# Kernel optimization log

Hardware: AMD Instinct MI355X
Metric: run time of the kernel (lower is better)

The kernel has to match this reference:

```python
import jax, jax.numpy as jnp
import numpy as np

# ---- static config (mirrors GptOssDecoderLayer init) ----
H = 1024      # hidden_size
HD = 64       # head_size
NQ = 16       # num_query_heads
NKV = 4       # num_key_value_heads
G = NQ // NKV # num_key_value_groups
E = 8         # num_experts
TOPK = 2      # experts_per_token
FFN = 1024    # expert intermediate (== hidden in GPT-OSS)
B, Q = 4, 128 # batch sequences, new query tokens per sequence
P, PS = 8, 128
S = P * PS    # kv length per sequence
T = B * Q     # total query tokens
SW = 128      # sliding window (layer_idx % 2 == 0 -> active)
LIMIT = 7.0   # swiglu_limit
ALPHA = 1.702
EPS = 1e-5
NEG = -1e30
SCALE = HD ** -0.5


def rmsnorm(x, w):
    return x * w * jax.lax.rsqrt(jnp.mean(x * x, axis=-1, keepdims=True) + EPS)


def setup_inputs() -> dict:
    key = jax.random.key(0)
    ks = jax.random.split(key, 16)
    hidden = jax.random.normal(ks[0], (T, H), jnp.float32)
    kv_cache = jax.random.normal(ks[1], (B * P, 2, PS, NKV, HD), jnp.float32)
    kv_page_indices = jnp.arange(B * P, dtype=jnp.int32).reshape(B, P)
    # additive causal mask: query q sits at absolute position S - Q + q
    qpos = S - Q + jnp.arange(Q)
    kpos = jnp.arange(S)
    causal = qpos[:, None] >= kpos[None, :]
    attention_mask = jnp.broadcast_to(
        jnp.where(causal, 0.0, NEG).astype(jnp.float32), (B, Q, S))
    sinks = 0.1 * jax.random.normal(ks[2], (NQ,), jnp.float32)
    w_qkv = jax.random.normal(ks[3], (H, HD * (NQ + 2 * NKV)), jnp.float32) / np.sqrt(H)
    b_qkv = jnp.zeros((HD * (NQ + 2 * NKV),), jnp.float32)
    w_o = jax.random.normal(ks[4], (NQ * HD, H), jnp.float32) / np.sqrt(NQ * HD)
    b_o = jnp.zeros((H,), jnp.float32)
    ln1_w = jnp.ones((H,), jnp.float32)
    ln2_w = jnp.ones((H,), jnp.float32)
    w_router = jax.random.normal(ks[5], (H, E), jnp.float32) / np.sqrt(H)
    b_router = jnp.zeros((E,), jnp.float32)
    w_gate_up = jax.random.normal(ks[6], (E, H, 2 * FFN), jnp.float32) / np.sqrt(H)
    b_gate_up = jnp.zeros((E, 2 * FFN), jnp.float32)
    w_down = jax.random.normal(ks[7], (E, FFN, H), jnp.float32) / np.sqrt(FFN)
    b_down = jnp.zeros((E, H), jnp.float32)
    return dict(hidden=hidden, kv_cache=kv_cache, attention_mask=attention_mask,
                kv_page_indices=kv_page_indices, sinks=sinks, w_qkv=w_qkv,
                b_qkv=b_qkv, w_o=w_o, b_o=b_o, ln1_w=ln1_w, ln2_w=ln2_w,
                w_router=w_router, b_router=b_router, w_gate_up=w_gate_up,
                b_gate_up=b_gate_up, w_down=w_down, b_down=b_down)


def reference(hidden, kv_cache, attention_mask, kv_page_indices, sinks,
              w_qkv, b_qkv, w_o, b_o, ln1_w, ln2_w, w_router, b_router,
              w_gate_up, b_gate_up, w_down, b_down):
    # ---- attention block ----
    x = rmsnorm(hidden, ln1_w)
    qkv = x @ w_qkv + b_qkv                       # [T, HD*(NQ+2*NKV)]
    q = qkv[:, :NQ * HD].reshape(B, Q, NQ, HD)
    k_new = qkv[:, NQ * HD:(NQ + NKV) * HD].reshape(B, Q, NKV, HD)
    v_new = qkv[:, (NQ + NKV) * HD:].reshape(B, Q, NKV, HD)
    # gather paged KV cache -> [B, S, NKV, HD]; write new tokens into tail slots
    pages = kv_cache[kv_page_indices]             # [B, P, 2, PS, NKV, HD]
    K = pages[:, :, 0].reshape(B, S, NKV, HD).at[:, S - Q:].set(k_new)
    V = pages[:, :, 1].reshape(B, S, NKV, HD).at[:, S - Q:].set(v_new)
    Kr = jnp.repeat(K, G, axis=2)                 # GQA expand -> [B, S, NQ, HD]
    Vr = jnp.repeat(V, G, axis=2)
    scores = jnp.einsum('bqhd,bshd->bhqs', q * SCALE, Kr) + attention_mask[:, None]
    # sliding-window (module trims pages outside the window; equivalent mask)
    qpos = S - Q + jnp.arange(Q)
    kpos = jnp.arange(S)
    win_ok = (qpos[:, None] - kpos[None, :]) < SW
    scores = jnp.where(win_ok[None, None], scores, NEG)
    m = jnp.max(scores, axis=-1)
    m = jnp.where(jnp.isinf(m) & (m < 0), 0.0, m)
    p = jnp.exp(scores - m[..., None])            # [B, NQ, Q, S]
    # attention sink joins the softmax denominator (online-softmax correction)
    denom = jnp.sum(p, axis=-1) + jnp.exp(sinks[None, :, None] - m)
    attn = jnp.einsum('bhqs,bshd->bhqd', p, Vr) / denom[..., None]
    attn = attn.transpose(0, 2, 1, 3).reshape(T, NQ * HD)
    h = hidden + attn @ w_o + b_o
    # ---- MoE block ----
    x2 = rmsnorm(h, ln2_w)
    logits = x2 @ w_router + b_router             # [T, E]
    vals, idx = jax.lax.top_k(logits, TOPK)
    wts = jax.nn.softmax(vals, axis=-1)
    comb = jnp.sum(jax.nn.one_hot(idx, E, dtype=x2.dtype) * wts[..., None], axis=1)
    gu = jnp.einsum('th,ehf->etf', x2, w_gate_up) + b_gate_up[:, None, :]
    gate = jnp.minimum(gu[..., 0::2], LIMIT)
    up = jnp.clip(gu[..., 1::2], -LIMIT, LIMIT)
    glu = gate * jax.nn.sigmoid(gate * ALPHA)
    eo = jnp.einsum('etf,efh->eth', (up + 1.0) * glu, w_down) + b_down[:, None, :]
    moe = jnp.einsum('te,eth->th', comb, eo)
    return h + moe
```

## Files before the change

### kernel.cpp

```cpp
#include <hip/hip_runtime.h>

constexpr int H    = 1024;
constexpr int HD   = 64;
constexpr int NQ   = 16;
constexpr int NKV  = 4;
constexpr int E_   = 8;
constexpr int FFN  = 1024;
constexpr int B_   = 4;
constexpr int Q_   = 128;
constexpr int P_   = 8;
constexpr int PS   = 128;
constexpr int S_   = P_ * PS;
constexpr int T_   = B_ * Q_;
constexpr int QKV_N = HD * (NQ + 2 * NKV);
constexpr float EPS   = 1e-5f;
constexpr float ALPHA = 1.702f;
constexpr float LIMIT = 7.0f;
constexpr float SCALE = 0.125f;

constexpr int MAXROWS = 1536;
constexpr int MAXTILES = 24;

typedef __attribute__((ext_vector_type(4))) float f32x4;
typedef __attribute__((ext_vector_type(8))) short s16x8;

__device__ __forceinline__ unsigned short f2bf(float f) {
    unsigned u = __float_as_uint(f);
    u += 0x7FFFu + ((u >> 16) & 1u);
    return (unsigned short)(u >> 16);
}

__global__ __launch_bounds__(256) void rmsnorm_kernel(const float* __restrict__ in,
                                                      const float* __restrict__ w,
                                                      unsigned short* __restrict__ outb,
                                                      int* __restrict__ cnt) {
    int t   = blockIdx.x;
    int tid = threadIdx.x;
    if (t == 0 && tid < E_) cnt[tid] = 0;
    float4 v = ((const float4*)(in + (size_t)t * H))[tid];
    float ss = v.x * v.x + v.y * v.y + v.z * v.z + v.w * v.w;
#pragma unroll
    for (int off = 32; off; off >>= 1) ss += __shfl_down(ss, off);
    __shared__ float partial[4];
    __shared__ float s_inv;
    if ((tid & 63) == 0) partial[tid >> 6] = ss;
    __syncthreads();
    if (tid == 0)
        s_inv = rsqrtf((partial[0] + partial[1] + partial[2] + partial[3]) * (1.0f / H) + EPS);
    __syncthreads();
    float inv = s_inv;
    float4 wv = ((const float4*)w)[tid];
    ushort4 ob;
    ob.x = f2bf(v.x * wv.x * inv); ob.y = f2bf(v.y * wv.y * inv);
    ob.z = f2bf(v.z * wv.z * inv); ob.w = f2bf(v.w * wv.w * inv);
    ((ushort4*)(outb + (size_t)t * H))[tid] = ob;
}

__global__ __launch_bounds__(256, 4) void gemm_dense_t(const unsigned short* __restrict__ Abf,
                                                       const float* __restrict__ W,
                                                       const float* __restrict__ bias,
                                                       const float* __restrict__ resid,
                                                       float* __restrict__ C,
                                                       float* __restrict__ Cdup, int N) {
    int nb = blockIdx.x, mb = blockIdx.y * 64;
    int tid = threadIdx.x;
    int w = tid >> 6, lane = tid & 63;
    int r16 = lane & 15, kq = lane >> 4;
    int skb = tid >> 5, sn = tid & 31;

    __shared__ unsigned short Wt[2][8][32][8];

    size_t sN = (size_t)N;
    const float* wsrc = W + (size_t)(skb * 8) * sN + nb * 32 + sn;
    const unsigned short* ap = Abf + (size_t)(mb + w * 16 + r16) * 1024 + kq * 8;

    float wr[2][8];
    s16x8 af[2][2];
    f32x4 acc[2] = {};

#pragma unroll
    for (int j = 0; j < 8; j++) wr[0][j] = wsrc[(size_t)j * sN];
    {
        s16x8 p;
#pragma unroll
        for (int j = 0; j < 8; j++) p[j] = (short)f2bf(wr[0][j]);
        *(s16x8*)&Wt[0][skb][sn][0] = p;
    }
#pragma unroll
    for (int j = 0; j < 8; j++) wr[1][j] = wsrc[(size_t)(64 + j) * sN];
#pragma unroll
    for (int ks = 0; ks < 2; ks++) af[0][ks] = *(const s16x8*)(ap + ks * 32);
    __syncthreads();

#pragma unroll
    for (int t = 0; t < 16; t++) {
        s16x8 b0[2], b1[2];
#pragma unroll
        for (int ks = 0; ks < 2; ks++) {
            b0[ks] = *(const s16x8*)&Wt[t & 1][ks * 4 + kq][r16][0];
            b1[ks] = *(const s16x8*)&Wt[t & 1][ks * 4 + kq][16 + r16][0];
        }
        if (t < 15) {
#pragma unroll
            for (int ks = 0; ks < 2; ks++)
                af[(t + 1) & 1][ks] = *(const s16x8*)(ap + (t + 1) * 64 + ks * 32);
        }
        if (t < 14) {
#pragma unroll
            for (int j = 0; j < 8; j++) wr[t & 1][j] = wsrc[(size_t)((t + 2) * 64 + j) * sN];
        }
#pragma unroll
        for (int ks = 0; ks < 2; ks++) {
            acc[0] = __builtin_amdgcn_mfma_f32_16x16x32_bf16(af[t & 1][ks], b0[ks], acc[0], 0, 0, 0);
            acc[1] = __builtin_amdgcn_mfma_f32_16x16x32_bf16(af[t & 1][ks], b1[ks], acc[1], 0, 0, 0);
        }
        if (t < 15) {
            s16x8 p;
#pragma unroll
            for (int j = 0; j < 8; j++) p[j] = (short)f2bf(wr[(t + 1) & 1][j]);
            *(s16x8*)&Wt[(t + 1) & 1][skb][sn][0] = p;
        }
        __syncthreads();
    }

    int row0 = mb + w * 16 + kq * 4;
#pragma unroll
    for (int nf = 0; nf < 2; nf++) {
        int col = nb * 32 + nf * 16 + r16;
        float bcol = bias[col];
#pragma unroll
        for (int r = 0; r < 4; r++) {
            int row = row0 + r;
            float v = acc[nf][r] + bcol;
            if (resid) v += resid[(size_t)row * sN + col];
            C[(size_t)row * sN + col] = v;
            if (Cdup) Cdup[(size_t)row * sN + col] = v;
        }
    }
}

__global__ __launch_bounds__(256) void attn_group_kernel(const float* __restrict__ qkv,
                                                         const float* __restrict__ kv_cache,
                                                         const int* __restrict__ page_idx,
                                                         const float* __restrict__ sinks,
                                                         unsigned short* __restrict__ attn_bf) {
    int blk = blockIdx.x;
    int kvh = blk & 3;
    int q   = (blk >> 2) & 127;
    int b   = blk >> 9;
    int t   = b * Q_ + q;
    int tid = threadIdx.x;
    int s_lo = S_ - Q_ - 127 + q;

    __shared__ __align__(16) float Vs[128][64];
    __shared__ __align__(16) float qs4[4][64];
    __shared__ float pv[4][128];
    __shared__ float sD[4];

#pragma unroll
    for (int r = 0; r < 8; r++) {
        int l = r * 256 + tid;
        int key = l >> 4, c = l & 15;
        int s = s_lo + key;
        const float* vp;
        if (s < S_ - Q_) {
            int page = page_idx[b * P_ + (s >> 7)];
            vp = kv_cache + (size_t)page * 65536 + 32768 + (size_t)(s & 127) * (NKV * HD) + kvh * HD;
        } else {
            vp = qkv + (size_t)(b * Q_ + (s - (S_ - Q_))) * QKV_N + (NQ + NKV) * HD + kvh * HD;
        }
        ((float4*)Vs[key])[c] = *(const float4*)(vp + c * 4);
    }
    {
        int hh = tid >> 6, d2 = tid & 63;
        qs4[hh][d2] = qkv[(size_t)t * QKV_N + (kvh * 4 + hh) * HD + d2];
    }
    __syncthreads();

    {
        int key = tid & 127, hp = tid >> 7;
        int s = s_lo + key;
        const float* kp;
        if (s < S_ - Q_) {
            int page = page_idx[b * P_ + (s >> 7)];
            kp = kv_cache + (size_t)page * 65536 + (size_t)(s & 127) * (NKV * HD) + kvh * HD;
        } else {
            kp = qkv + (size_t)(b * Q_ + (s - (S_ - Q_))) * QKV_N + NQ * HD + kvh * HD;
        }
        const float4* kp4 = (const float4*)kp;
        const float4* q0p = (const float4*)qs4[hp * 2];
        const float4* q1p = (const float4*)qs4[hp * 2 + 1];
        float sc0 = 0.f, sc1 = 0.f;
#pragma unroll
        for (int d4 = 0; d4 < 16; d4++) {
            float4 kk = kp4[d4];
            float4 q0 = q0p[d4], q1 = q1p[d4];
            sc0 += q0.x * kk.x + q0.y * kk.y + q0.z * kk.z + q0.w * kk.w;
            sc1 += q1.x * kk.x + q1.y * kk.y + q1.z * kk.z + q1.w * kk.w;
        }
        pv[hp * 2][key]     = sc0 * SCALE;
        pv[hp * 2 + 1][key] = sc1 * SCALE;
    }
    __syncthreads();

    {
        int wv = tid >> 6, lane = tid & 63;
        float a0 = pv[wv][lane], a1 = pv[wv][lane + 64];
        float m = fmaxf(a0, a1);
#pragma unroll
        for (int off = 32; off; off >>= 1) m = fmaxf(m, __shfl_xor(m, off));
        float p0 = __expf(a0 - m), p1 = __expf(a1 - m);
        float l = p0 + p1;
#pragma unroll
        for (int off = 32; off; off >>= 1) l += __shfl_xor(l, off);
        pv[wv][lane] = p0;
        pv[wv][lane + 64] = p1;
        if (lane == 0) sD[wv] = l + __expf(sinks[kvh * 4 + wv] - m);
    }
    __syncthreads();

    {
        int hh = tid >> 6, d2 = tid & 63;
        float a0 = 0.f, a1 = 0.f, a2 = 0.f, a3 = 0.f;
#pragma unroll 4
        for (int i = 0; i < 128; i += 4) {
            a0 += pv[hh][i]     * Vs[i][d2];
            a1 += pv[hh][i + 1] * Vs[i + 1][d2];
            a2 += pv[hh][i + 2] * Vs[i + 2][d2];
            a3 += pv[hh][i + 3] * Vs[i + 3][d2];
        }
        float acc = ((a0 + a1) + (a2 + a3)) / sD[hh];
        attn_bf[(size_t)t * (NQ * HD) + (kvh * 4 + hh) * HD + d2] = f2bf(acc);
    }
}

__global__ __launch_bounds__(256) void rms_router_kernel(const float* __restrict__ hbuf,
                                                         const float* __restrict__ ln2w,
                                                         const float* __restrict__ w_router,
                                                         const float* __restrict__ b_router,
                                                         unsigned short* __restrict__ x2bf,
                                                         int* __restrict__ ridx,
                                                         float* __restrict__ rwt,
                                                         int* __restrict__ cnt) {
    int t = blockIdx.x;
    int tid = threadIdx.x;
    float4 v = ((const float4*)(hbuf + (size_t)t * H))[tid];
    float ss = v.x * v.x + v.y * v.y + v.z * v.z + v.w * v.w;
#pragma unroll
    for (int off = 32; off; off >>= 1) ss += __shfl_down(ss, off);
    __shared__ float partial[4];
    __shared__ float s_inv;
    if ((tid & 63) == 0) partial[tid >> 6] = ss;
    __syncthreads();
    if (tid == 0)
        s_inv = rsqrtf((partial[0] + partial[1] + partial[2] + partial[3]) * (1.0f / H) + EPS);
    __syncthreads();
    float inv = s_inv;
    float4 wv = ((const float4*)ln2w)[tid];
    float4 o;
    o.x = v.x * wv.x * inv; o.y = v.y * wv.y * inv;
    o.z = v.z * wv.z * inv; o.w = v.w * wv.w * inv;
    ushort4 ob;
    ob.x = f2bf(o.x); ob.y = f2bf(o.y); ob.z = f2bf(o.z); ob.w = f2bf(o.w);
    ((ushort4*)(x2bf + (size_t)t * H))[tid] = ob;

    const float4* wr = (const float4*)(w_router + (size_t)tid * 4 * E_);
    float p[E_];
    {
        float4 r0a = wr[0], r0b = wr[1];
        float4 r1a = wr[2], r1b = wr[3];
        float4 r2a = wr[4], r2b = wr[5];
        float4 r3a = wr[6], r3b = wr[7];
        p[0] = o.x * r0a.x + o.y * r1a.x + o.z * r2a.x + o.w * r3a.x;
        p[1] = o.x * r0a.y + o.y * r1a.y + o.z * r2a.y + o.w * r3a.y;
        p[2] = o.x * r0a.z + o.y * r1a.z + o.z * r2a.z + o.w * r3a.z;
        p[3] = o.x * r0a.w + o.y * r1a.w + o.z * r2a.w + o.w * r3a.w;
        p[4] = o.x * r0b.x + o.y * r1b.x + o.z * r2b.x + o.w * r3b.x;
        p[5] = o.x * r0b.y + o.y * r1b.y + o.z * r2b.y + o.w * r3b.y;
        p[6] = o.x * r0b.z + o.y * r1b.z + o.z * r2b.z + o.w * r3b.z;
        p[7] = o.x * r0b.w + o.y * r1b.w + o.z * r2b.w + o.w * r3b.w;
    }
    __shared__ float wsum[4][E_];
    int wv2 = tid >> 6, lane = tid & 63;
#pragma unroll
    for (int e = 0; e < E_; e++) {
        float r = p[e];
#pragma unroll
        for (int off = 32; off; off >>= 1) r += __shfl_xor(r, off);
        if (lane == 0) wsum[wv2][e] = r;
    }
    __syncthreads();
    __shared__ float logits[E_];
    if (tid < E_)
        logits[tid] = wsum[0][tid] + wsum[1][tid] + wsum[2][tid] + wsum[3][tid] + b_router[tid];
    __syncthreads();
    if (tid == 0) {
        int i0 = 0; float v0 = logits[0];
        for (int ee = 1; ee < E_; ee++)
            if (logits[ee] > v0) { v0 = logits[ee]; i0 = ee; }
        int i1 = -1; float v1 = -3.4e38f;
        for (int ee = 0; ee < E_; ee++)
            if (ee != i0 && logits[ee] > v1) { v1 = logits[ee]; i1 = ee; }
        float w0 = 1.0f / (1.0f + __expf(v1 - v0));
        ridx[t * 2] = i0; ridx[t * 2 + 1] = i1;
        rwt[t * 2] = w0;  rwt[t * 2 + 1] = 1.0f - w0;
        atomicAdd(&cnt[i0], 1);
        atomicAdd(&cnt[i1], 1);
    }
}

__global__ __launch_bounds__(256) void plumb_kernel(const int* __restrict__ cnt,
                                                    const int* __restrict__ ridx,
                                                    int* __restrict__ poff,
                                                    int* __restrict__ list,
                                                    int* __restrict__ tmap) {
    __shared__ int lpos[E_], lpoff[E_];
    int tid = threadIdx.x;
    if (tid == 0) {
        int run = 0, it = 0;
        for (int e = 0; e < E_; e++) {
            lpoff[e] = run; poff[e] = run;
            int pc = (cnt[e] + 63) & ~63;
            for (int tl = 0; tl < (pc >> 6); tl++) tmap[1 + it++] = (e << 5) | tl;
            run += pc;
        }
        tmap[0] = it;
    }
    if (tid < E_) lpos[tid] = 0;
    __syncthreads();
    for (int i = tid; i < 2 * T_; i += 256) {
        int e = ridx[i];
        int pp = atomicAdd(&lpos[e], 1);
        list[lpoff[e] + pp] = i;
    }
}

__global__ __launch_bounds__(256, 4) void moe_gateup_t(const unsigned short* __restrict__ x2bf,
                                                       const int* __restrict__ list,
                                                       const int* __restrict__ cnt,
                                                       const int* __restrict__ poff,
                                                       const int* __restrict__ tmap,
                                                       const float* __restrict__ wgu,
                                                       const float* __restrict__ bgu,
                                                       unsigned short* __restrict__ act_bf) {
    if ((int)blockIdx.y >= tmap[0]) return;
    int v0m = tmap[1 + blockIdx.y];
    int e = v0m >> 5, tl = v0m & 31;
    int n = cnt[e];
    int base = poff[e];
    int nb = blockIdx.x;
    int tid = threadIdx.x;
    int w = tid >> 6, lane = tid & 63;
    int r16 = lane & 15, kq = lane >> 4;
    int skb = tid >> 5, sn = tid & 31;

    __shared__ unsigned short Wt[2][8][32][8];

    const float* wsrc = wgu + (size_t)e * (1024 * 2048) + (size_t)(skb * 8) * 2048 + nb * 32 + sn;
    int rr0 = tl * 64 + w * 16 + r16;
    int t2a = (rr0 < n) ? list[base + rr0] : list[base];
    const unsigned short* ap = x2bf + (size_t)(t2a >> 1) * 1024 + kq * 8;

    float wr[2][8];
    s16x8 af[2][2];
    f32x4 acc[2] = {};

#pragma unroll
    for (int j = 0; j < 8; j++) wr[0][j] = wsrc[(size_t)j * 2048];
    {
        s16x8 p;
#pragma unroll
        for (int j = 0; j < 8; j++) p[j] = (short)f2bf(wr[0][j]);
        *(s16x8*)&Wt[0][skb][sn][0] = p;
    }
#pragma unroll
    for (int j = 0; j < 8; j++) wr[1][j] = wsrc[(size_t)(64 + j) * 2048];
#pragma unroll
    for (int ks = 0; ks < 2; ks++) af[0][ks] = *(const s16x8*)(ap + ks * 32);
    __syncthreads();

#pragma unroll
    for (int t = 0; t < 16; t++) {
        s16x8 b0[2], b1[2];
#pragma unroll
        for (int ks = 0; ks < 2; ks++) {
            b0[ks] = *(const s16x8*)&Wt[t & 1][ks * 4 + kq][r16][0];
            b1[ks] = *(const s16x8*)&Wt[t & 1][ks * 4 + kq][16 + r16][0];
        }
        if (t < 15) {
#pragma unroll
            for (int ks = 0; ks < 2; ks++)
                af[(t + 1) & 1][ks] = *(const s16x8*)(ap + (t + 1) * 64 + ks * 32);
        }
        if (t < 14) {
#pragma unroll
            for (int j = 0; j < 8; j++) wr[t & 1][j] = wsrc[(size_t)((t + 2) * 64 + j) * 2048];
        }
#pragma unroll
        for (int ks = 0; ks < 2; ks++) {
            acc[0] = __builtin_amdgcn_mfma_f32_16x16x32_bf16(af[t & 1][ks], b0[ks], acc[0], 0, 0, 0);
            acc[1] = __builtin_amdgcn_mfma_f32_16x16x32_bf16(af[t & 1][ks], b1[ks], acc[1], 0, 0, 0);
        }
        if (t < 15) {
            s16x8 p;
#pragma unroll
            for (int j = 0; j < 8; j++) p[j] = (short)f2bf(wr[(t + 1) & 1][j]);
            *(s16x8*)&Wt[(t + 1) & 1][skb][sn][0] = p;
        }
        __syncthreads();
    }

    int parity = r16 & 1;
#pragma unroll
    for (int nf = 0; nf < 2; nf++) {
        int gucol = nb * 32 + nf * 16 + r16;
        float bb = bgu[(size_t)e * 2048 + gucol];
#pragma unroll
        for (int r = 0; r < 4; r++) {
            float v = acc[nf][r] + bb;
            float o = __shfl_xor(v, 1);
            if (!parity) {
                float g = fminf(v, LIMIT);
                float u = fminf(fmaxf(o, -LIMIT), LIMIT);
                float glu = g / (1.0f + __expf(-ALPHA * g));
                int rr = tl * 64 + w * 16 + kq * 4 + r;
                if (rr < n)
                    act_bf[(size_t)(base + rr) * FFN + (gucol >> 1)] = f2bf((u + 1.0f) * glu);
            }
        }
    }
}

__global__ __launch_bounds__(256, 4) void moe_down_t(const unsigned short* __restrict__ act_bf,
                                                     const int* __restrict__ list,
                                                     const int* __restrict__ cnt,
                                                     const int* __restrict__ poff,
                                                     const int* __restrict__ tmap,
                                                     const float* __restrict__ rwt,
                                                     const float* __restrict__ wdn,
                                                     const float* __restrict__ b_down,
                                                     float* __restrict__ out) {
    if ((int)blockIdx.y >= tmap[0]) return;
    int v0m = tmap[1 + blockIdx.y];
    int e = v0m >> 5, tl = v0m & 31;
    int n = cnt[e];
    int base = poff[e];
    int nb = blockIdx.x;
    int z  = blockIdx.z;
    int tid = threadIdx.x;
    int w = tid >> 6, lane = tid & 63;
    int r16 = lane & 15, kq = lane >> 4;
    int skb = tid >> 5, sn = tid & 31;

    __shared__ unsigned short Wt[2][8][32][8];

    const float* wsrc = wdn + (size_t)e * (1024 * 1024) + (size_t)(z * 512 + skb * 8) * 1024 + nb * 32 + sn;
    const unsigned short* ap = act_bf + (size_t)(base + tl * 64 + w * 16 + r16) * 1024 + z * 512 + kq * 8;

    float wr[2][8];
    s16x8 af[2][2];
    f32x4 acc[2] = {};

#pragma unroll
    for (int j = 0; j < 8; j++) wr[0][j] = wsrc[(size_t)j * 1024];
    {
        s16x8 p;
#pragma unroll
        for (int j = 0; j < 8; j++) p[j] = (short)f2bf(wr[0][j]);
        *(s16x8*)&Wt[0][skb][sn][0] = p;
    }
#pragma unroll
    for (int j = 0; j < 8; j++) wr[1][j] = wsrc[(size_t)(64 + j) * 1024];
#pragma unroll
    for (int ks = 0; ks < 2; ks++) af[0][ks] = *(const s16x8*)(ap + ks * 32);
    __syncthreads();

#pragma unroll
    for (int t = 0; t < 8; t++) {
        s16x8 b0[2], b1[2];
#pragma unroll
        for (int ks = 0; ks < 2; ks++) {
            b0[ks] = *(const s16x8*)&Wt[t & 1][ks * 4 + kq][r16][0];
            b1[ks] = *(const s16x8*)&Wt[t & 1][ks * 4 + kq][16 + r16][0];
        }
        if (t < 7) {
#pragma unroll
            for (int ks = 0; ks < 2; ks++)
                af[(t + 1) & 1][ks] = *(const s16x8*)(ap + (t + 1) * 64 + ks * 32);
        }
        if (t < 6) {
#pragma unroll
            for (int j = 0; j < 8; j++) wr[t & 1][j] = wsrc[(size_t)((t + 2) * 64 + j) * 1024];
        }
#pragma unroll
        for (int ks = 0; ks < 2; ks++) {
            acc[0] = __builtin_amdgcn_mfma_f32_16x16x32_bf16(af[t & 1][ks], b0[ks], acc[0], 0, 0, 0);
            acc[1] = __builtin_amdgcn_mfma_f32_16x16x32_bf16(af[t & 1][ks], b1[ks], acc[1], 0, 0, 0);
        }
        if (t < 7) {
            s16x8 p;
#pragma unroll
            for (int j = 0; j < 8; j++) p[j] = (short)f2bf(wr[(t + 1) & 1][j]);
            *(s16x8*)&Wt[(t + 1) & 1][skb][sn][0] = p;
        }
        __syncthreads();
    }

#pragma unroll
    for (int r = 0; r < 4; r++) {
        int rr = tl * 64 + w * 16 + kq * 4 + r;
        if (rr < n) {
            int t2 = list[base + rr];
            float sc = rwt[t2];
            float* op = out + (size_t)(t2 >> 1) * H;
#pragma unroll
            for (int nf = 0; nf < 2; nf++) {
                int col = nb * 32 + nf * 16 + r16;
                float v = acc[nf][r] + (z == 0 ? b_down[(size_t)e * 1024 + col] : 0.0f);
                atomicAdd(op + col, sc * v);
            }
        }
    }
}

extern "C" void kernel_launch(void* const* d_in, const int* in_sizes, int n_in,
                              void* d_out, int out_size, void* d_ws, size_t ws_size,
                              hipStream_t stream) {
    const float* hidden          = (const float*)d_in[0];
    const float* kv_cache        = (const float*)d_in[1];
    const int*   kv_page_indices = (const int*)d_in[3];
    const float* sinks           = (const float*)d_in[4];
    const float* w_qkv           = (const float*)d_in[5];
    const float* b_qkv           = (const float*)d_in[6];
    const float* w_o             = (const float*)d_in[7];
    const float* b_o             = (const float*)d_in[8];
    const float* ln1_w           = (const float*)d_in[9];
    const float* ln2_w           = (const float*)d_in[10];
    const float* w_router        = (const float*)d_in[11];
    const float* b_router        = (const float*)d_in[12];
    const float* w_gate_up       = (const float*)d_in[13];
    const float* b_gate_up       = (const float*)d_in[14];
    const float* w_down          = (const float*)d_in[15];
    const float* b_down          = (const float*)d_in[16];
    float* out = (float*)d_out;

    char* base = (char*)d_ws;
    float* qkv   = (float*)base;                       base += (size_t)T_ * QKV_N * 4;
    float* hbuf  = (float*)base;                       base += (size_t)T_ * H * 4;
    unsigned short* x_bf    = (unsigned short*)base;   base += (size_t)T_ * H * 2;
    unsigned short* x2_bf   = (unsigned short*)base;   base += (size_t)T_ * H * 2;
    unsigned short* attn_bf = (unsigned short*)base;   base += (size_t)T_ * NQ * HD * 2;
    unsigned short* act_bf  = (unsigned short*)base;   base += (size_t)(MAXROWS + 128) * FFN * 2;
    float* rwt  = (float*)base;                        base += 2 * T_ * 4;
    int*   ridx = (int*)base;                          base += 2 * T_ * 4;
    int*   cnt  = (int*)base;                          base += E_ * 4;
    int*   poff = (int*)base;                          base += E_ * 4;
    int*   list = (int*)base;                          base += MAXROWS * 4;
    int*   tmap = (int*)base;                          base += (1 + MAXTILES + 7) * 4;

    rmsnorm_kernel<<<T_, 256, 0, stream>>>(hidden, ln1_w, x_bf, cnt);
    gemm_dense_t<<<dim3(QKV_N / 32, T_ / 64), 256, 0, stream>>>(
        x_bf, w_qkv, b_qkv, nullptr, qkv, nullptr, QKV_N);
    attn_group_kernel<<<B_ * Q_ * NKV, 256, 0, stream>>>(qkv, kv_cache, kv_page_indices, sinks, attn_bf);
    gemm_dense_t<<<dim3(H / 32, T_ / 64), 256, 0, stream>>>(
        attn_bf, w_o, b_o, hidden, hbuf, out, H);
    rms_router_kernel<<<T_, 256, 0, stream>>>(hbuf, ln2_w, w_router, b_router,
                                              x2_bf, ridx, rwt, cnt);
    plumb_kernel<<<1, 256, 0, stream>>>(cnt, ridx, poff, list, tmap);
    moe_gateup_t<<<dim3(FFN * 2 / 32, MAXTILES), 256, 0, stream>>>(
        x2_bf, list, cnt, poff, tmap, w_gate_up, b_gate_up, act_bf);
    moe_down_t<<<dim3(H / 32, MAXTILES, 2), 256, 0, stream>>>(
        act_bf, list, cnt, poff, tmap, rwt, w_down, b_down, out);
}
```

Before: 274.7 us.

## Deepen weight prefetch pipeline to four stages with explicit LDS barriers

Restructures the three bf16 MFMA GEMM kernels (dense, MoE gate-up, MoE down) so global weight loads are issued four k-tiles ahead, using rotating register buffers and named ping-pong LDS tiles. __syncthreads is replaced by a custom barrier that waits only on LDS counters, so in-flight global loads are not drained at each step. The occupancy hint is dropped from launch_bounds to make room for the extra registers. This aims to hide global memory latency on the fp32 weight stream, at the cost of higher register pressure and possibly lower occupancy.

Result: no change. 278.0 us (+1.2%).

```diff
diff --git a/kernel.cpp b/kernel.cpp
--- a/kernel.cpp
+++ b/kernel.cpp
@@ -30,6 +30,11 @@
     return (unsigned short)(u >> 16);
 }
 
+__device__ __forceinline__ void lds_barrier() {
+    asm volatile("s_waitcnt lgkmcnt(0)" ::: "memory");
+    __builtin_amdgcn_s_barrier();
+}
+
 __global__ __launch_bounds__(256) void rmsnorm_kernel(const float* __restrict__ in,
                                                       const float* __restrict__ w,
                                                       unsigned short* __restrict__ outb,
@@ -56,74 +61,88 @@
     ((ushort4*)(outb + (size_t)t * H))[tid] = ob;
 }
 
-__global__ __launch_bounds__(256, 4) void gemm_dense_t(const unsigned short* __restrict__ Abf,
-                                                       const float* __restrict__ W,
-                                                       const float* __restrict__ bias,
-                                                       const float* __restrict__ resid,
-                                                       float* __restrict__ C,
-                                                       float* __restrict__ Cdup, int N) {
+#define GPHASE(LDSR, LDSW, WRW, WRI, TI, NT, AFD0, AFD1, TA, AFS0, AFS1, STRIDE)      \
+    {                                                                                  \
+        s16x8 b00 = *(const s16x8*)&LDSR[kq][r16][0];                                  \
+        s16x8 b01 = *(const s16x8*)&LDSR[kq][16 + r16][0];                             \
+        s16x8 b10 = *(const s16x8*)&LDSR[4 + kq][r16][0];                              \
+        s16x8 b11 = *(const s16x8*)&LDSR[4 + kq][16 + r16][0];                         \
+        if (TA < NT) {                                                                 \
+            AFD0 = *(const s16x8*)(ap + (TA) * 64);                                    \
+            AFD1 = *(const s16x8*)(ap + (TA) * 64 + 32);                               \
+        }                                                                              \
+        if (TI < NT) {                                                                 \
+            _Pragma("unroll")                                                          \
+            for (int j = 0; j < 8; j++) WRI[j] = wsrc[(size_t)((TI) * 64 + j) * STRIDE]; \
+        }                                                                              \
+        acc0 = __builtin_amdgcn_mfma_f32_16x16x32_bf16(AFS0, b00, acc0, 0, 0, 0);      \
+        acc1 = __builtin_amdgcn_mfma_f32_16x16x32_bf16(AFS0, b01, acc1, 0, 0, 0);      \
+        acc0 = __builtin_amdgcn_mfma_f32_16x16x32_bf16(AFS1, b10, acc0, 0, 0, 0);      \
+        acc1 = __builtin_amdgcn_mfma_f32_16x16x32_bf16(AFS1, b11, acc1, 0, 0, 0);      \
+        if (TI - 3 < NT) {                                                             \
+            s16x8 p;                                                                   \
+            _Pragma("unroll")                                                          \
+            for (int j = 0; j < 8; j++) p[j] = (short)f2bf(WRW[j]);                    \
+            *(s16x8*)&LDSW[skb][sn][0] = p;                                            \
+        }                                                                              \
+        lds_barrier();                                                                 \
+    }
+
+#define GPROLOGUE(NT, STRIDE)                                                          \
+    float wr0[8], wr1[8], wr2[8], wr3[8], wrP[8];                                      \
+    s16x8 afA0, afA1, afB0, afB1;                                                      \
+    f32x4 acc0 = {}, acc1 = {};                                                        \
+    _Pragma("unroll")                                                                  \
+    for (int j = 0; j < 8; j++) wrP[j] = wsrc[(size_t)j * STRIDE];                     \
+    _Pragma("unroll")                                                                  \
+    for (int j = 0; j < 8; j++) wr0[j] = wsrc[(size_t)(64 + j) * STRIDE];              \
+    if (2 < NT) { _Pragma("unroll")                                                    \
+        for (int j = 0; j < 8; j++) wr1[j] = wsrc[(size_t)(128 + j) * STRIDE]; }       \
+    if (3 < NT) { _Pragma("unroll")                                                    \
+        for (int j = 0; j < 8; j++) wr2[j] = wsrc[(size_t)(192 + j) * STRIDE]; }       \
+    {                                                                                  \
+        s16x8 p;                                                                       \
+        _Pragma("unroll")                                                              \
+        for (int j = 0; j < 8; j++) p[j] = (short)f2bf(wrP[j]);                        \
+        *(s16x8*)&WtA[skb][sn][0] = p;                                                 \
+    }                                                                                  \
+    afA0 = *(const s16x8*)(ap);                                                        \
+    afA1 = *(const s16x8*)(ap + 32);                                                   \
+    lds_barrier();
+
+#define GQUAD(T, NT, STRIDE)                                                           \
+    GPHASE(WtA, WtB, wr0, wr3, (T) + 4, NT, afB0, afB1, (T) + 1, afA0, afA1, STRIDE)   \
+    GPHASE(WtB, WtA, wr1, wr0, (T) + 5, NT, afA0, afA1, (T) + 2, afB0, afB1, STRIDE)   \
+    GPHASE(WtA, WtB, wr2, wr1, (T) + 6, NT, afB0, afB1, (T) + 3, afA0, afA1, STRIDE)   \
+    GPHASE(WtB, WtA, wr3, wr2, (T) + 7, NT, afA0, afA1, (T) + 4, afB0, afB1, STRIDE)
+
+__global__ __launch_bounds__(256) void gemm_dense_t(const unsigned short* __restrict__ Abf,
+                                                    const float* __restrict__ W,
+                                                    const float* __restrict__ bias,
+                                                    const float* __restrict__ resid,
+                                                    float* __restrict__ C,
+                                                    float* __restrict__ Cdup, int N) {
     int nb = blockIdx.x, mb = blockIdx.y * 64;
     int tid = threadIdx.x;
     int w = tid >> 6, lane = tid & 63;
     int r16 = lane & 15, kq = lane >> 4;
     int skb = tid >> 5, sn = tid & 31;
 
-    __shared__ unsigned short Wt[2][8][32][8];
+    __shared__ unsigned short WtA[8][32][8];
+    __shared__ unsigned short WtB[8][32][8];
 
     size_t sN = (size_t)N;
     const float* wsrc = W + (size_t)(skb * 8) * sN + nb * 32 + sn;
     const unsigned short* ap = Abf + (size_t)(mb + w * 16 + r16) * 1024 + kq * 8;
 
-    float wr[2][8];
-    s16x8 af[2][2];
-    f32x4 acc[2] = {};
-
-#pragma unroll
-    for (int j = 0; j < 8; j++) wr[0][j] = wsrc[(size_t)j * sN];
-    {
-        s16x8 p;
-#pragma unroll
-        for (int j = 0; j < 8; j++) p[j] = (short)f2bf(wr[0][j]);
-        *(s16x8*)&Wt[0][skb][sn][0] = p;
-    }
-#pragma unroll
-    for (int j = 0; j < 8; j++) wr[1][j] = wsrc[(size_t)(64 + j) * sN];
-#pragma unroll
-    for (int ks = 0; ks < 2; ks++) af[0][ks] = *(const s16x8*)(ap + ks * 32);
-    __syncthreads();
-
-#pragma unroll
-    for (int t = 0; t < 16; t++) {
-        s16x8 b0[2], b1[2];
-#pragma unroll
-        for (int ks = 0; ks < 2; ks++) {
-            b0[ks] = *(const s16x8*)&Wt[t & 1][ks * 4 + kq][r16][0];
-            b1[ks] = *(const s16x8*)&Wt[t & 1][ks * 4 + kq][16 + r16][0];
-        }
-        if (t < 15) {
-#pragma unroll
-            for (int ks = 0; ks < 2; ks++)
-                af[(t + 1) & 1][ks] = *(const s16x8*)(ap + (t + 1) * 64 + ks * 32);
-        }
-        if (t < 14) {
-#pragma unroll
-            for (int j = 0; j < 8; j++) wr[t & 1][j] = wsrc[(size_t)((t + 2) * 64 + j) * sN];
-        }
-#pragma unroll
-        for (int ks = 0; ks < 2; ks++) {
-            acc[0] = __builtin_amdgcn_mfma_f32_16x16x32_bf16(af[t & 1][ks], b0[ks], acc[0], 0, 0, 0);
-            acc[1] = __builtin_amdgcn_mfma_f32_16x16x32_bf16(af[t & 1][ks], b1[ks], acc[1], 0, 0, 0);
-        }
-        if (t < 15) {
-            s16x8 p;
-#pragma unroll
-            for (int j = 0; j < 8; j++) p[j] = (short)f2bf(wr[(t + 1) & 1][j]);
-            *(s16x8*)&Wt[(t + 1) & 1][skb][sn][0] = p;
-        }
-        __syncthreads();
+    GPROLOGUE(16, sN)
+#pragma unroll
+    for (int i = 0; i < 4; i++) {
+        GQUAD(4 * i, 16, sN)
     }
 
     int row0 = mb + w * 16 + kq * 4;
+    f32x4 accs[2] = {acc0, acc1};
 #pragma unroll
     for (int nf = 0; nf < 2; nf++) {
         int col = nb * 32 + nf * 16 + r16;
@@ -131,7 +150,7 @@
 #pragma unroll
         for (int r = 0; r < 4; r++) {
             int row = row0 + r;
-            float v = acc[nf][r] + bcol;
+            float v = accs[nf][r] + bcol;
             if (resid) v += resid[(size_t)row * sN + col];
             C[(size_t)row * sN + col] = v;
             if (Cdup) Cdup[(size_t)row * sN + col] = v;
@@ -335,14 +354,14 @@
     }
 }
 
-__global__ __launch_bounds__(256, 4) void moe_gateup_t(const unsigned short* __restrict__ x2bf,
-                                                       const int* __restrict__ list,
-                                                       const int* __restrict__ cnt,
-                                                       const int* __restrict__ poff,
-                                                       const int* __restrict__ tmap,
-                                                       const float* __restrict__ wgu,
-                                                       const float* __restrict__ bgu,
-                                                       unsigned short* __restrict__ act_bf) {
+__global__ __launch_bounds__(256) void moe_gateup_t(const unsigned short* __restrict__ x2bf,
+                                                    const int* __restrict__ list,
+                                                    const int* __restrict__ cnt,
+                                                    const int* __restrict__ poff,
+                                                    const int* __restrict__ tmap,
+                                                    const float* __restrict__ wgu,
+                                                    const float* __restrict__ bgu,
+                                                    unsigned short* __restrict__ act_bf) {
     if ((int)blockIdx.y >= tmap[0]) return;
     int v0m = tmap[1 + blockIdx.y];
     int e = v0m >> 5, tl = v0m & 31;
@@ -354,70 +373,29 @@
     int r16 = lane & 15, kq = lane >> 4;
     int skb = tid >> 5, sn = tid & 31;
 
-    __shared__ unsigned short Wt[2][8][32][8];
+    __shared__ unsigned short WtA[8][32][8];
+    __shared__ unsigned short WtB[8][32][8];
 
     const float* wsrc = wgu + (size_t)e * (1024 * 2048) + (size_t)(skb * 8) * 2048 + nb * 32 + sn;
     int rr0 = tl * 64 + w * 16 + r16;
     int t2a = (rr0 < n) ? list[base + rr0] : list[base];
     const unsigned short* ap = x2bf + (size_t)(t2a >> 1) * 1024 + kq * 8;
 
-    float wr[2][8];
-    s16x8 af[2][2];
-    f32x4 acc[2] = {};
-
-#pragma unroll
-    for (int j = 0; j < 8; j++) wr[0][j] = wsrc[(size_t)j * 2048];
-    {
-        s16x8 p;
-#pragma unroll
-        for (int j = 0; j < 8; j++) p[j] = (short)f2bf(wr[0][j]);
-        *(s16x8*)&Wt[0][skb][sn][0] = p;
-    }
-#pragma unroll
-    for (int j = 0; j < 8; j++) wr[1][j] = wsrc[(size_t)(64 + j) * 2048];
-#pragma unroll
-    for (int ks = 0; ks < 2; ks++) af[0][ks] = *(const s16x8*)(ap + ks * 32);
-    __syncthreads();
-
-#pragma unroll
-    for (int t = 0; t < 16; t++) {
-        s16x8 b0[2], b1[2];
-#pragma unroll
-        for (int ks = 0; ks < 2; ks++) {
-            b0[ks] = *(const s16x8*)&Wt[t & 1][ks * 4 + kq][r16][0];
-            b1[ks] = *(const s16x8*)&Wt[t & 1][ks * 4 + kq][16 + r16][0];
-        }
-        if (t < 15) {
-#pragma unroll
-            for (int ks = 0; ks < 2; ks++)
-                af[(t + 1) & 1][ks] = *(const s16x8*)(ap + (t + 1) * 64 + ks * 32);
-        }
-        if (t < 14) {
-#pragma unroll
-            for (int j = 0; j < 8; j++) wr[t & 1][j] = wsrc[(size_t)((t + 2) * 64 + j) * 2048];
-        }
-#pragma unroll
-        for (int ks = 0; ks < 2; ks++) {
-            acc[0] = __builtin_amdgcn_mfma_f32_16x16x32_bf16(af[t & 1][ks], b0[ks], acc[0], 0, 0, 0);
-            acc[1] = __builtin_amdgcn_mfma_f32_16x16x32_bf16(af[t & 1][ks], b1[ks], acc[1], 0, 0, 0);
-        }
-        if (t < 15) {
-            s16x8 p;
-#pragma unroll
-            for (int j = 0; j < 8; j++) p[j] = (short)f2bf(wr[(t + 1) & 1][j]);
-            *(s16x8*)&Wt[(t + 1) & 1][skb][sn][0] = p;
-        }
-        __syncthreads();
+    GPROLOGUE(16, 2048)
+#pragma unroll
+    for (int i = 0; i < 4; i++) {
+        GQUAD(4 * i, 16, 2048)
     }
 
     int parity = r16 & 1;
+    f32x4 accs[2] = {acc0, acc1};
 #pragma unroll
     for (int nf = 0; nf < 2; nf++) {
         int gucol = nb * 32 + nf * 16 + r16;
         float bb = bgu[(size_t)e * 2048 + gucol];
 #pragma unroll
         for (int r = 0; r < 4; r++) {
-            float v = acc[nf][r] + bb;
+            float v = accs[nf][r] + bb;
             float o = __shfl_xor(v, 1);
             if (!parity) {
                 float g = fminf(v, LIMIT);
@@ -431,15 +409,15 @@
     }
 }
 
-__global__ __launch_bounds__(256, 4) void moe_down_t(const unsigned short* __restrict__ act_bf,
-                                                     const int* __restrict__ list,
-                                                     const int* __restrict__ cnt,
-                                                     const int* __restrict__ poff,
-                                                     const int* __restrict__ tmap,
-                                                     const float* __restrict__ rwt,
-                                                     const float* __restrict__ wdn,
-                                                     const float* __restrict__ b_down,
-                                                     float* __restrict__ out) {
+__global__ __launch_bounds__(256) void moe_down_t(const unsigned short* __restrict__ act_bf,
+                                                  const int* __restrict__ list,
+                                                  const int* __restrict__ cnt,
+                                                  const int* __restrict__ poff,
+                                                  const int* __restrict__ tmap,
+                                                  const float* __restrict__ rwt,
+                                                  const float* __restrict__ wdn,
+                                                  const float* __restrict__ b_down,
+                                                  float* __restrict__ out) {
     if ((int)blockIdx.y >= tmap[0]) return;
     int v0m = tmap[1 + blockIdx.y];
     int e = v0m >> 5, tl = v0m & 31;
@@ -452,60 +430,19 @@
     int r16 = lane & 15, kq = lane >> 4;
     int skb = tid >> 5, sn = tid & 31;
 
-    __shared__ unsigned short Wt[2][8][32][8];
+    __shared__ unsigned short WtA[8][32][8];
+    __shared__ unsigned short WtB[8][32][8];
 
     const float* wsrc = wdn + (size_t)e * (1024 * 1024) + (size_t)(z * 512 + skb * 8) * 1024 + nb * 32 + sn;
     const unsigned short* ap = act_bf + (size_t)(base + tl * 64 + w * 16 + r16) * 1024 + z * 512 + kq * 8;
 
-    float wr[2][8];
-    s16x8 af[2][2];
-    f32x4 acc[2] = {};
-
-#pragma unroll
-    for (int j = 0; j < 8; j++) wr[0][j] = wsrc[(size_t)j * 1024];
-    {
-        s16x8 p;
-#pragma unroll
-        for (int j = 0; j < 8; j++) p[j] = (short)f2bf(wr[0][j]);
-        *(s16x8*)&Wt[0][skb][sn][0] = p;
-    }
-#pragma unroll
-    for (int j = 0; j < 8; j++) wr[1][j] = wsrc[(size_t)(64 + j) * 1024];
-#pragma unroll
-    for (int ks = 0; ks < 2; ks++) af[0][ks] = *(const s16x8*)(ap + ks * 32);
-    __syncthreads();
-
-#pragma unroll
-    for (int t = 0; t < 8; t++) {
-        s16x8 b0[2], b1[2];
-#pragma unroll
-        for (int ks = 0; ks < 2; ks++) {
-            b0[ks] = *(const s16x8*)&Wt[t & 1][ks * 4 + kq][r16][0];
-            b1[ks] = *(const s16x8*)&Wt[t & 1][ks * 4 + kq][16 + r16][0];
-        }
-        if (t < 7) {
-#pragma unroll
-            for (int ks = 0; ks < 2; ks++)
-                af[(t + 1) & 1][ks] = *(const s16x8*)(ap + (t + 1) * 64 + ks * 32);
-        }
-        if (t < 6) {
-#pragma unroll
-            for (int j = 0; j < 8; j++) wr[t & 1][j] = wsrc[(size_t)((t + 2) * 64 + j) * 1024];
-        }
-#pragma unroll
-        for (int ks = 0; ks < 2; ks++) {
-            acc[0] = __builtin_amdgcn_mfma_f32_16x16x32_bf16(af[t & 1][ks], b0[ks], acc[0], 0, 0, 0);
-            acc[1] = __builtin_amdgcn_mfma_f32_16x16x32_bf16(af[t & 1][ks], b1[ks], acc[1], 0, 0, 0);
-        }
-        if (t < 7) {
-            s16x8 p;
-#pragma unroll
-            for (int j = 0; j < 8; j++) p[j] = (short)f2bf(wr[(t + 1) & 1][j]);
-            *(s16x8*)&Wt[(t + 1) & 1][skb][sn][0] = p;
-        }
-        __syncthreads();
-    }
-
+    GPROLOGUE(8, 1024)
+#pragma unroll
+    for (int i = 0; i < 2; i++) {
+        GQUAD(4 * i, 8, 1024)
+    }
+
+    f32x4 accs[2] = {acc0, acc1};
 #pragma unroll
     for (int r = 0; r < 4; r++) {
         int rr = tl * 64 + w * 16 + kq * 4 + r;
@@ -516,7 +453,7 @@
 #pragma unroll
             for (int nf = 0; nf < 2; nf++) {
                 int col = nb * 32 + nf * 16 + r16;
-                float v = acc[nf][r] + (z == 0 ? b_down[(size_t)e * 1024 + col] : 0.0f);
+                float v = accs[nf][r] + (z == 0 ? b_down[(size_t)e * 1024 + col] : 0.0f);
                 atomicAdd(op + col, sc * v);
             }
         }
```
